# Performance work log

Hardware: AMD Instinct MI355X
Metric: run time of the kernel (lower is better)

Reference implementation:

```python
import jax, jax.numpy as jnp
import numpy as np

# Model dims: N = polynomial degree, RANK = CP rank, HxW image, S = flattened size
N, RANK, H, W = 4, 128, 256, 256
S = H * W
B = 32
EPS = 1e-5  # torch BatchNorm2d default eps


def setup_inputs() -> dict:
    key = jax.random.key(0)
    ks = jax.random.split(key, 4)
    x = jax.random.normal(ks[0], (B, 1, H, W), dtype=jnp.float32)
    # PolyLayer (PolyGAN CCP) parameters: per-degree factors U_n [S, RANK],
    # output projection C [S, RANK], output bias beta [S]
    U = jax.random.normal(ks[1], (N, S, RANK), dtype=jnp.float32) * 0.02
    C = jax.random.normal(ks[2], (S, RANK), dtype=jnp.float32) * 0.02
    beta = jax.random.normal(ks[3], (S,), dtype=jnp.float32) * 0.02
    # BatchNorm2d(1) affine params (torch default init: weight=1, bias=0)
    gamma = jnp.ones((1,), dtype=jnp.float32)
    bn_bias = jnp.zeros((1,), dtype=jnp.float32)
    return {"x": x, "U": U, "C": C, "beta": beta, "gamma": gamma, "bn_bias": bn_bias}


def reference(x, U, C, beta, gamma, bn_bias):
    b = x.shape[0]
    # BatchNorm2d(num_features=1), training mode: biased batch stats over (N,H,W)
    mean = jnp.mean(x, axis=(0, 2, 3), keepdims=True)
    var = jnp.var(x, axis=(0, 2, 3), keepdims=True)
    xn = (x - mean) * jax.lax.rsqrt(var + EPS)
    xn = xn * gamma.reshape(1, -1, 1, 1) + bn_bias.reshape(1, -1, 1, 1)
    # Flatten each sample: [B, S]. The torch Generator applies PolyLayer
    # per-sample across Python threads; here it is one batched call.
    z = xn.reshape(b, S)
    # CCP polynomial: t_n = U_n^T z for each degree -> [N, B, RANK]
    t = jnp.einsum('bs,nsr->nbr', z, U)
    h = t[0]
    for n in range(1, N):  # fixed small degree loop (structural, not data dim)
        h = t[n] * h + h   # h_n = (U_n^T z) * h_{n-1} + h_{n-1}
    out = h @ C.T + beta   # project back to image space: [B, S]
    return out.reshape(b, 1, H, W)
```

## Files before the change

### kernel.cpp

```cpp
#include <hip/hip_runtime.h>

#define SDIM 65536
#define BDIM 32
#define RDIM 128
#define NDEG 4
#define NCHUNK 512
#define CHUNK_S (SDIM / NCHUNK)
#define NSTEP (CHUNK_S / 16)
#define MTOT (BDIM * SDIM)
#define EPS_BN 1e-5f
#define NSTATB 512

typedef float f32x4 __attribute__((ext_vector_type(4)));

__global__ void k_stats(const float* __restrict__ x, float* __restrict__ partial) {
    __shared__ float s_sum[256];
    __shared__ float s_sq[256];
    int tid = threadIdx.x;
    int gid = blockIdx.x * 256 + tid;
    int stride = gridDim.x * 256;
    float sum = 0.f, sq = 0.f;
    const float4* x4 = (const float4*)x;
    for (int i = gid; i < MTOT / 4; i += stride) {
        float4 v = x4[i];
        sum += (v.x + v.y) + (v.z + v.w);
        sq  += (v.x * v.x + v.y * v.y) + (v.z * v.z + v.w * v.w);
    }
    s_sum[tid] = sum; s_sq[tid] = sq;
    __syncthreads();
    for (int off = 128; off > 0; off >>= 1) {
        if (tid < off) { s_sum[tid] += s_sum[tid + off]; s_sq[tid] += s_sq[tid + off]; }
        __syncthreads();
    }
    if (tid == 0) { partial[blockIdx.x * 2] = s_sum[0]; partial[blockIdx.x * 2 + 1] = s_sq[0]; }
}

__global__ void k_stats_fin(const float* __restrict__ partial, float* __restrict__ stats) {
    __shared__ float s_sum[256];
    __shared__ float s_sq[256];
    int tid = threadIdx.x;
    float sum = partial[tid * 2] + partial[(tid + 256) * 2];
    float sq  = partial[tid * 2 + 1] + partial[(tid + 256) * 2 + 1];
    s_sum[tid] = sum; s_sq[tid] = sq;
    __syncthreads();
    for (int off = 128; off > 0; off >>= 1) {
        if (tid < off) { s_sum[tid] += s_sum[tid + off]; s_sq[tid] += s_sq[tid + off]; }
        __syncthreads();
    }
    if (tid == 0) { stats[0] = s_sum[0]; stats[1] = s_sq[0]; }
}

__global__ void __launch_bounds__(256) k_norm_t(const float* __restrict__ x,
                                                const float* __restrict__ gamma,
                                                const float* __restrict__ bnb,
                                                const float* __restrict__ stats,
                                                float* __restrict__ zT) {
    __shared__ float lds[64][33];
    int tid = threadIdx.x;
    int s0 = blockIdx.x * 64;
    float mean = stats[0] * (1.f / MTOT);
    float var  = stats[1] * (1.f / MTOT) - mean * mean;
    float istd = rsqrtf(var + EPS_BN);
    float a  = gamma[0] * istd;
    float c0 = bnb[0] - mean * a;

    int sl = tid & 63, bq = tid >> 6;
#pragma unroll
    for (int k = 0; k < 8; ++k) {
        int b = k * 4 + bq;
        lds[sl][b] = fmaf(a, x[(size_t)b * SDIM + s0 + sl], c0);
    }
    __syncthreads();
    int bl = tid & 31, sq = tid >> 5;
#pragma unroll
    for (int k = 0; k < 8; ++k) {
        int s = k * 8 + sq;
        zT[(size_t)(s0 + s) * BDIM + bl] = lds[s][bl];
    }
}

#define FMA16(zz, uu) \
    acc[0][0]=fmaf((zz).x,(uu).x,acc[0][0]); acc[0][1]=fmaf((zz).x,(uu).y,acc[0][1]); \
    acc[0][2]=fmaf((zz).x,(uu).z,acc[0][2]); acc[0][3]=fmaf((zz).x,(uu).w,acc[0][3]); \
    acc[1][0]=fmaf((zz).y,(uu).x,acc[1][0]); acc[1][1]=fmaf((zz).y,(uu).y,acc[1][1]); \
    acc[1][2]=fmaf((zz).y,(uu).z,acc[1][2]); acc[1][3]=fmaf((zz).y,(uu).w,acc[1][3]); \
    acc[2][0]=fmaf((zz).z,(uu).x,acc[2][0]); acc[2][1]=fmaf((zz).z,(uu).y,acc[2][1]); \
    acc[2][2]=fmaf((zz).z,(uu).z,acc[2][2]); acc[2][3]=fmaf((zz).z,(uu).w,acc[2][3]); \
    acc[3][0]=fmaf((zz).w,(uu).x,acc[3][0]); acc[3][1]=fmaf((zz).w,(uu).y,acc[3][1]); \
    acc[3][2]=fmaf((zz).w,(uu).z,acc[3][2]); acc[3][3]=fmaf((zz).w,(uu).w,acc[3][3]);

#define GLL(gp, lp) __builtin_amdgcn_global_load_lds( \
    (const __attribute__((address_space(1))) void*)(gp), \
    (__attribute__((address_space(3))) void*)(lp), 16, 0, 0)

__global__ void __launch_bounds__(256) k_gemm_t(const float* __restrict__ zT,
                                                const float* __restrict__ U,
                                                float* __restrict__ t_part) {
    __shared__ float z_lds[CHUNK_S * BDIM];
    __shared__ float u_lds[2][16 * RDIM];
    int tid  = threadIdx.x;
    int p    = tid & 31;
    int o    = tid >> 5;
    int wv   = tid >> 6;
    int ln   = tid & 63;
    int chunk = blockIdx.x;
    int n     = blockIdx.y;
    int s0 = chunk * CHUNK_S;

    {
        const float4* src4 = (const float4*)(zT + (size_t)s0 * BDIM);
        float4* dst4 = (float4*)z_lds;
#pragma unroll
        for (int i = 0; i < (CHUNK_S * BDIM / 4) / 256; ++i)
            dst4[i * 256 + tid] = src4[i * 256 + tid];
    }

    const float* Ut = U + (size_t)n * SDIM * RDIM + (size_t)s0 * RDIM;

    {
        const float* gp = Ut + (size_t)(4 * wv) * RDIM + ln * 4;
        float* lp = &u_lds[0][4 * wv * RDIM];
        GLL(gp, lp);
        GLL(gp + 256, lp + 256);
    }
    __syncthreads();

    float acc[4][4];
#pragma unroll
    for (int j = 0; j < 4; ++j)
#pragma unroll
        for (int k = 0; k < 4; ++k) acc[j][k] = 0.f;

    for (int t = 0; t < NSTEP; ++t) {
        if (t + 1 < NSTEP) {
            const float* gp = Ut + (size_t)((t + 1) * 16 + 4 * wv) * RDIM + ln * 4;
            float* lp = &u_lds[(t + 1) & 1][4 * wv * RDIM];
            GLL(gp, lp);
            GLL(gp + 256, lp + 256);
        }
        const float* ub = u_lds[t & 1];
        const float* zb = z_lds + (size_t)(t * 16) * BDIM;
#pragma unroll
        for (int rr = 0; rr < 16; ++rr) {
            f32x4 u4 = *(const f32x4*)(ub + rr * RDIM + 4 * p);
            f32x4 z4 = *(const f32x4*)(zb + rr * BDIM + 4 * o);
            FMA16(z4, u4)
        }
        __syncthreads();
    }

    float* outp = t_part + ((size_t)n * NCHUNK + chunk) * (BDIM * RDIM);
#pragma unroll
    for (int j = 0; j < 4; ++j) {
        int b = o * 4 + j;
        *(float4*)(outp + b * RDIM + 4 * p) =
            make_float4(acc[j][0], acc[j][1], acc[j][2], acc[j][3]);
    }
}

__global__ void __launch_bounds__(256) k_reduce_h(const float* __restrict__ t_part,
                                                  float* __restrict__ h) {
    __shared__ float lds[NDEG][8][32];
    int tid = threadIdx.x;
    int il = tid & 31;
    int cg = tid >> 5;
    int i0 = blockIdx.x * 32;

#pragma unroll
    for (int n = 0; n < NDEG; ++n) {
        float s = 0.f;
#pragma unroll 8
        for (int k = 0; k < 64; ++k) {
            int c = cg * 64 + k;
            s += t_part[(size_t)(n * NCHUNK + c) * (BDIM * RDIM) + i0 + il];
        }
        lds[n][cg][il] = s;
    }
    __syncthreads();
    if (tid < 32) {
        float t[NDEG];
#pragma unroll
        for (int n = 0; n < NDEG; ++n) {
            float s = 0.f;
#pragma unroll
            for (int g = 0; g < 8; ++g) s += lds[n][g][il];
            t[n] = s;
        }
        float hh = t[0];
#pragma unroll
        for (int n = 1; n < NDEG; ++n) hh = fmaf(t[n], hh, hh);
        h[i0 + il] = hh;
    }
}

__global__ void __launch_bounds__(256) k_out(const float* __restrict__ h,
                                             const float* __restrict__ Cm,
                                             const float* __restrict__ beta,
                                             float* __restrict__ out) {
    int tid = threadIdx.x;
    int s   = (blockIdx.x >> 1) * 64 + (tid & 63);
    int bg  = __builtin_amdgcn_readfirstlane((blockIdx.x & 1) * 4 + (tid >> 6));
    int b0  = bg * 4;

    float acc[4] = {0.f, 0.f, 0.f, 0.f};
    const float4* Cr = (const float4*)(Cm + (size_t)s * RDIM);
    const float* hb = h + b0 * RDIM;

#pragma unroll 8
    for (int rc = 0; rc < RDIM / 4; ++rc) {
        float4 c = Cr[rc];
#pragma unroll
        for (int j = 0; j < 4; ++j) {
            const float* hr = hb + j * RDIM + rc * 4;
            float a = acc[j];
            a = fmaf(c.x, hr[0], a);
            a = fmaf(c.y, hr[1], a);
            a = fmaf(c.z, hr[2], a);
            a = fmaf(c.w, hr[3], a);
            acc[j] = a;
        }
    }
    float bt = beta[s];
#pragma unroll
    for (int j = 0; j < 4; ++j)
        out[(size_t)(b0 + j) * SDIM + s] = acc[j] + bt;
}

extern "C" void kernel_launch(void* const* d_in, const int* in_sizes, int n_in,
                              void* d_out, int out_size, void* d_ws, size_t ws_size,
                              hipStream_t stream) {
    const float* x     = (const float*)d_in[0];
    const float* U     = (const float*)d_in[1];
    const float* Cm    = (const float*)d_in[2];
    const float* beta  = (const float*)d_in[3];
    const float* gamma = (const float*)d_in[4];
    const float* bnb   = (const float*)d_in[5];
    float* out = (float*)d_out;

    char* ws = (char*)d_ws;
    size_t off = 0;
    float* stats   = (float*)(ws + off); off += 256;
    float* partial = (float*)(ws + off); off += NSTATB * 2 * 4;
    float* zT      = (float*)(ws + off); off += (size_t)BDIM * SDIM * 4;
    float* t_part  = (float*)(ws + off); off += (size_t)NDEG * NCHUNK * BDIM * RDIM * 4;
    float* h       = (float*)(ws + off); off += (size_t)BDIM * RDIM * 4;

    k_stats<<<NSTATB, 256, 0, stream>>>(x, partial);
    k_stats_fin<<<1, 256, 0, stream>>>(partial, stats);
    k_norm_t<<<SDIM / 64, 256, 0, stream>>>(x, gamma, bnb, stats, zT);
    dim3 g3(NCHUNK, NDEG);
    k_gemm_t<<<g3, 256, 0, stream>>>(zT, U, t_part);
    k_reduce_h<<<128, 256, 0, stream>>>(t_part, h);
    k_out<<<2048, 256, 0, stream>>>(h, Cm, beta, out);
}
```

Before: 107.9 us.

## Retile GEMM threads as 4x8 with split-K halves and two-stage reduction

The first GEMM now gives each thread a 4x8 output tile and splits the 16-row K step between two 128-thread halves, which are combined through LDS at the end. The partial-output layout is changed to chunk-major. The single cross-chunk reduction kernel is replaced by a two-stage float4 reduction (512→64→1) so that more blocks take part and reads are coalesced. The aim is more FMAs per LDS load and a faster partial reduction, at the cost of an extra launch and a 4 MB intermediate buffer.

```diff
diff --git a/kernel.cpp b/kernel.cpp
--- a/kernel.cpp
+++ b/kernel.cpp
@@ -5,13 +5,12 @@
 #define RDIM 128
 #define NDEG 4
 #define NCHUNK 512
-#define CHUNK_S (SDIM / NCHUNK)
+#define CHUNK_S 128
 #define NSTEP (CHUNK_S / 16)
 #define MTOT (BDIM * SDIM)
 #define EPS_BN 1e-5f
 #define NSTATB 512
-
-typedef float f32x4 __attribute__((ext_vector_type(4)));
+#define TSLICE (NDEG * BDIM * RDIM)
 
 __global__ void k_stats(const float* __restrict__ x, float* __restrict__ partial) {
     __shared__ float s_sum[256];
@@ -79,16 +78,6 @@
     }
 }
 
-#define FMA16(zz, uu) \
-    acc[0][0]=fmaf((zz).x,(uu).x,acc[0][0]); acc[0][1]=fmaf((zz).x,(uu).y,acc[0][1]); \
-    acc[0][2]=fmaf((zz).x,(uu).z,acc[0][2]); acc[0][3]=fmaf((zz).x,(uu).w,acc[0][3]); \
-    acc[1][0]=fmaf((zz).y,(uu).x,acc[1][0]); acc[1][1]=fmaf((zz).y,(uu).y,acc[1][1]); \
-    acc[1][2]=fmaf((zz).y,(uu).z,acc[1][2]); acc[1][3]=fmaf((zz).y,(uu).w,acc[1][3]); \
-    acc[2][0]=fmaf((zz).z,(uu).x,acc[2][0]); acc[2][1]=fmaf((zz).z,(uu).y,acc[2][1]); \
-    acc[2][2]=fmaf((zz).z,(uu).z,acc[2][2]); acc[2][3]=fmaf((zz).z,(uu).w,acc[2][3]); \
-    acc[3][0]=fmaf((zz).w,(uu).x,acc[3][0]); acc[3][1]=fmaf((zz).w,(uu).y,acc[3][1]); \
-    acc[3][2]=fmaf((zz).w,(uu).z,acc[3][2]); acc[3][3]=fmaf((zz).w,(uu).w,acc[3][3]);
-
 #define GLL(gp, lp) __builtin_amdgcn_global_load_lds( \
     (const __attribute__((address_space(1))) void*)(gp), \
     (__attribute__((address_space(3))) void*)(lp), 16, 0, 0)
@@ -98,99 +87,136 @@
                                                 float* __restrict__ t_part) {
     __shared__ float z_lds[CHUNK_S * BDIM];
     __shared__ float u_lds[2][16 * RDIM];
-    int tid  = threadIdx.x;
-    int p    = tid & 31;
-    int o    = tid >> 5;
-    int wv   = tid >> 6;
-    int ln   = tid & 63;
+    int tid = threadIdx.x;
+    int pl  = tid >> 7;
+    int t7  = tid & 127;
+    int o   = t7 >> 4;
+    int p   = t7 & 15;
     int chunk = blockIdx.x;
     int n     = blockIdx.y;
-    int s0 = chunk * CHUNK_S;
+    size_t s0 = (size_t)chunk * CHUNK_S;
 
     {
-        const float4* src4 = (const float4*)(zT + (size_t)s0 * BDIM);
-        float4* dst4 = (float4*)z_lds;
+        const float4* src = (const float4*)(zT + s0 * BDIM);
+        float4* dst = (float4*)z_lds;
 #pragma unroll
         for (int i = 0; i < (CHUNK_S * BDIM / 4) / 256; ++i)
-            dst4[i * 256 + tid] = src4[i * 256 + tid];
-    }
-
-    const float* Ut = U + (size_t)n * SDIM * RDIM + (size_t)s0 * RDIM;
-
+            dst[i * 256 + tid] = src[i * 256 + tid];
+    }
+
+    const float* Ut = U + (size_t)n * SDIM * RDIM + s0 * RDIM;
     {
-        const float* gp = Ut + (size_t)(4 * wv) * RDIM + ln * 4;
-        float* lp = &u_lds[0][4 * wv * RDIM];
+        const float* gp = Ut + tid * 4;
+        float* lp = &u_lds[0][0] + tid * 4;
         GLL(gp, lp);
-        GLL(gp + 256, lp + 256);
-    }
-    __syncthreads();
-
-    float acc[4][4];
+        GLL(gp + 1024, lp + 1024);
+    }
+    __syncthreads();
+
+    float acc[4][8];
 #pragma unroll
     for (int j = 0; j < 4; ++j)
 #pragma unroll
-        for (int k = 0; k < 4; ++k) acc[j][k] = 0.f;
+        for (int k = 0; k < 8; ++k) acc[j][k] = 0.f;
 
     for (int t = 0; t < NSTEP; ++t) {
         if (t + 1 < NSTEP) {
-            const float* gp = Ut + (size_t)((t + 1) * 16 + 4 * wv) * RDIM + ln * 4;
-            float* lp = &u_lds[(t + 1) & 1][4 * wv * RDIM];
+            const float* gp = Ut + (size_t)(t + 1) * 16 * RDIM + tid * 4;
+            float* lp = &u_lds[(t + 1) & 1][0] + tid * 4;
             GLL(gp, lp);
-            GLL(gp + 256, lp + 256);
-        }
-        const float* ub = u_lds[t & 1];
-        const float* zb = z_lds + (size_t)(t * 16) * BDIM;
-#pragma unroll
-        for (int rr = 0; rr < 16; ++rr) {
-            f32x4 u4 = *(const f32x4*)(ub + rr * RDIM + 4 * p);
-            f32x4 z4 = *(const f32x4*)(zb + rr * BDIM + 4 * o);
-            FMA16(z4, u4)
+            GLL(gp + 1024, lp + 1024);
+        }
+        const float* ubase = u_lds[t & 1];
+        const float* zbase = z_lds + (size_t)t * 16 * BDIM;
+#pragma unroll
+        for (int rr = 0; rr < 8; ++rr) {
+            int rl = 8 * pl + rr;
+            float4 z4  = *(const float4*)(zbase + rl * BDIM + 4 * o);
+            float4 ua4 = *(const float4*)(ubase + rl * RDIM + 4 * p);
+            float4 ub4 = *(const float4*)(ubase + rl * RDIM + 64 + 4 * p);
+#pragma unroll
+            for (int j = 0; j < 4; ++j) {
+                float zj = (j == 0) ? z4.x : (j == 1) ? z4.y : (j == 2) ? z4.z : z4.w;
+                acc[j][0] = fmaf(zj, ua4.x, acc[j][0]);
+                acc[j][1] = fmaf(zj, ua4.y, acc[j][1]);
+                acc[j][2] = fmaf(zj, ua4.z, acc[j][2]);
+                acc[j][3] = fmaf(zj, ua4.w, acc[j][3]);
+                acc[j][4] = fmaf(zj, ub4.x, acc[j][4]);
+                acc[j][5] = fmaf(zj, ub4.y, acc[j][5]);
+                acc[j][6] = fmaf(zj, ub4.z, acc[j][6]);
+                acc[j][7] = fmaf(zj, ub4.w, acc[j][7]);
+            }
         }
         __syncthreads();
     }
 
-    float* outp = t_part + ((size_t)n * NCHUNK + chunk) * (BDIM * RDIM);
-#pragma unroll
-    for (int j = 0; j < 4; ++j) {
-        int b = o * 4 + j;
-        *(float4*)(outp + b * RDIM + 4 * p) =
-            make_float4(acc[j][0], acc[j][1], acc[j][2], acc[j][3]);
-    }
-}
-
-__global__ void __launch_bounds__(256) k_reduce_h(const float* __restrict__ t_part,
+    float* cm = &u_lds[0][0];
+    if (pl == 1) {
+#pragma unroll
+        for (int j = 0; j < 4; ++j)
+#pragma unroll
+            for (int k = 0; k < 8; ++k)
+                cm[t7 * 32 + j * 8 + k] = acc[j][k];
+    }
+    __syncthreads();
+    if (pl == 0) {
+        float* outp = t_part + ((size_t)chunk * NDEG + n) * (BDIM * RDIM);
+#pragma unroll
+        for (int j = 0; j < 4; ++j) {
+#pragma unroll
+            for (int k = 0; k < 8; ++k) acc[j][k] += cm[t7 * 32 + j * 8 + k];
+            int b = 4 * o + j;
+            *(float4*)(outp + b * RDIM + 4 * p) =
+                make_float4(acc[j][0], acc[j][1], acc[j][2], acc[j][3]);
+            *(float4*)(outp + b * RDIM + 64 + 4 * p) =
+                make_float4(acc[j][4], acc[j][5], acc[j][6], acc[j][7]);
+        }
+    }
+}
+
+__global__ void __launch_bounds__(256) k_reduce_a(const float* __restrict__ t_part,
+                                                  float* __restrict__ t_mid) {
+    int tid = threadIdx.x;
+    int j = blockIdx.x;
+    int strip = blockIdx.y;
+    const float4* tp4 = (const float4*)t_part;
+    float4* tm4 = (float4*)t_mid;
+#pragma unroll
+    for (int e = 0; e < 4; ++e) {
+        int idx = strip * 1024 + e * 256 + tid;
+        float4 s = make_float4(0.f, 0.f, 0.f, 0.f);
+#pragma unroll
+        for (int c = 0; c < 8; ++c) {
+            float4 v = tp4[(size_t)(8 * j + c) * (TSLICE / 4) + idx];
+            s.x += v.x; s.y += v.y; s.z += v.z; s.w += v.w;
+        }
+        tm4[(size_t)j * (TSLICE / 4) + idx] = s;
+    }
+}
+
+__global__ void __launch_bounds__(256) k_reduce_b(const float* __restrict__ t_mid,
                                                   float* __restrict__ h) {
-    __shared__ float lds[NDEG][8][32];
-    int tid = threadIdx.x;
-    int il = tid & 31;
-    int cg = tid >> 5;
-    int i0 = blockIdx.x * 32;
-
-#pragma unroll
-    for (int n = 0; n < NDEG; ++n) {
-        float s = 0.f;
-#pragma unroll 8
-        for (int k = 0; k < 64; ++k) {
-            int c = cg * 64 + k;
-            s += t_part[(size_t)(n * NCHUNK + c) * (BDIM * RDIM) + i0 + il];
-        }
-        lds[n][cg][il] = s;
-    }
-    __syncthreads();
-    if (tid < 32) {
-        float t[NDEG];
+    int i3q = blockIdx.x * 256 + threadIdx.x;
+    const float4* tm4 = (const float4*)t_mid;
+    float4 tn[NDEG];
+#pragma unroll
+    for (int n = 0; n < NDEG; ++n) tn[n] = make_float4(0.f, 0.f, 0.f, 0.f);
+    for (int j = 0; j < 64; ++j) {
 #pragma unroll
         for (int n = 0; n < NDEG; ++n) {
-            float s = 0.f;
-#pragma unroll
-            for (int g = 0; g < 8; ++g) s += lds[n][g][il];
-            t[n] = s;
-        }
-        float hh = t[0];
-#pragma unroll
-        for (int n = 1; n < NDEG; ++n) hh = fmaf(t[n], hh, hh);
-        h[i0 + il] = hh;
-    }
+            float4 v = tm4[(size_t)j * (TSLICE / 4) + n * 1024 + i3q];
+            tn[n].x += v.x; tn[n].y += v.y; tn[n].z += v.z; tn[n].w += v.w;
+        }
+    }
+    float4 hh = tn[0];
+#pragma unroll
+    for (int n = 1; n < NDEG; ++n) {
+        hh.x = fmaf(tn[n].x, hh.x, hh.x);
+        hh.y = fmaf(tn[n].y, hh.y, hh.y);
+        hh.z = fmaf(tn[n].z, hh.z, hh.z);
+        hh.w = fmaf(tn[n].w, hh.w, hh.w);
+    }
+    ((float4*)h)[i3q] = hh;
 }
 
 __global__ void __launch_bounds__(256) k_out(const float* __restrict__ h,
@@ -242,7 +268,8 @@
     float* stats   = (float*)(ws + off); off += 256;
     float* partial = (float*)(ws + off); off += NSTATB * 2 * 4;
     float* zT      = (float*)(ws + off); off += (size_t)BDIM * SDIM * 4;
-    float* t_part  = (float*)(ws + off); off += (size_t)NDEG * NCHUNK * BDIM * RDIM * 4;
+    float* t_part  = (float*)(ws + off); off += (size_t)NCHUNK * TSLICE * 4;
+    float* t_mid   = (float*)(ws + off); off += (size_t)64 * TSLICE * 4;
     float* h       = (float*)(ws + off); off += (size_t)BDIM * RDIM * 4;
 
     k_stats<<<NSTATB, 256, 0, stream>>>(x, partial);
@@ -250,6 +277,8 @@
     k_norm_t<<<SDIM / 64, 256, 0, stream>>>(x, gamma, bnb, stats, zT);
     dim3 g3(NCHUNK, NDEG);
     k_gemm_t<<<g3, 256, 0, stream>>>(zT, U, t_part);
-    k_reduce_h<<<128, 256, 0, stream>>>(t_part, h);
+    dim3 g4(64, 4);
+    k_reduce_a<<<g4, 256, 0, stream>>>(t_part, t_mid);
+    k_reduce_b<<<4, 256, 0, stream>>>(t_mid, h);
     k_out<<<2048, 256, 0, stream>>>(h, Cm, beta, out);
 }
```

Result: slower. 117.4 us (+8.9%).
